# Kernel optimization log

Measured on AMD Instinct MI355X. Metric: run time of the kernel, lower is better.

## Reference

```python
import jax, jax.numpy as jnp
import numpy as np
from jax import lax

B, C, H = 16384, 512, 1024
IN = C + 4  # context + prev_delta(2) + heading(2)
LN_EPS = 1e-5


def _layernorm(x, g, b):
    mu = x.mean(-1, keepdims=True)
    var = ((x - mu) ** 2).mean(-1, keepdims=True)
    return (x - mu) * lax.rsqrt(var + LN_EPS) * g + b


def setup_inputs() -> dict:
    key = jax.random.key(0)
    ks = jax.random.split(key, 16)
    s = lambda fan_in: 1.0 / np.sqrt(fan_in)
    return {
        "context": jax.random.normal(ks[0], (B, C), jnp.float32),
        "last_pos": jax.random.normal(ks[1], (B, 2), jnp.float32),
        "last_delta": jax.random.normal(ks[2], (B, 2), jnp.float32) * 0.1,
        "Wh": jax.random.normal(ks[3], (H, C), jnp.float32) * s(C),
        "bh": jnp.zeros((H,), jnp.float32),
        "Wc": jax.random.normal(ks[4], (H, C), jnp.float32) * s(C),
        "bc": jnp.zeros((H,), jnp.float32),
        "W_ih": jax.random.normal(ks[5], (4 * H, IN), jnp.float32) * s(H),
        "b_ih": jax.random.normal(ks[6], (4 * H,), jnp.float32) * s(H),
        "W_hh": jax.random.normal(ks[7], (4 * H, H), jnp.float32) * s(H),
        "b_hh": jax.random.normal(ks[8], (4 * H,), jnp.float32) * s(H),
        "ln_g": jnp.ones((H,), jnp.float32),
        "ln_b": jnp.zeros((H,), jnp.float32),
        "W1": jax.random.normal(ks[9], (H, H), jnp.float32) * s(H),
        "b1": jnp.zeros((H,), jnp.float32),
        "W2": jax.random.normal(ks[10], (2, H), jnp.float32) * s(H),
        "b2": jnp.zeros((2,), jnp.float32),
        "pred_len": 60,
    }


def reference(context, last_pos, last_delta, Wh, bh, Wc, bc, W_ih, b_ih, W_hh, b_hh,
              ln_g, ln_b, W1, b1, W2, b2, pred_len):
    hidden = jnp.tanh(context @ Wh.T + bh)
    cell = jnp.tanh(context @ Wc.T + bc)
    # context part of LSTM input gates is constant across steps: precompute
    gates_ctx = context @ W_ih[:, :C].T + b_ih  # [B, 4H]
    W_extra = W_ih[:, C:]  # [4H, 4]

    def step(carry, _):
        h, c, pos, pd = carry
        heading = pd / jnp.maximum(jnp.linalg.norm(pd, axis=-1, keepdims=True), 1e-6)
        extra = jnp.concatenate([pd, heading], axis=-1)  # [B,4]
        gates = gates_ctx + extra @ W_extra.T + h @ W_hh.T + b_hh
        i, f, g, o = jnp.split(gates, 4, axis=-1)
        c = jax.nn.sigmoid(f) * c + jax.nn.sigmoid(i) * jnp.tanh(g)
        h = jax.nn.sigmoid(o) * jnp.tanh(c)
        y = _layernorm(h, ln_g, ln_b)  # dropout is identity in eval
        y = jax.nn.gelu(y @ W1.T + b1, approximate=False)
        delta = y @ W2.T + b2  # [B,2]
        pos = pos + delta
        return (h, c, pos, delta), pos

    _, outs = lax.scan(step, (hidden, cell, last_pos, last_delta), None, length=pred_len)
    return jnp.swapaxes(outs, 0, 1)  # [B, pred_len, 2]
```

## Files before the change

### kernel.cpp

```cpp
#include <hip/hip_runtime.h>
#include <math.h>

constexpr int BATCH = 16384;
constexpr int CDIM  = 512;
constexpr int HDIM  = 1024;
constexpr int GDIM  = 4096;
constexpr int TSTEP = 60;
constexpr float LOSC  = 2048.0f;
constexpr float ILOSC = 1.0f / 2048.0f;

typedef _Float16 half_t;
typedef _Float16 halfx8 __attribute__((ext_vector_type(8)));
typedef _Float16 halfx4 __attribute__((ext_vector_type(4)));
typedef float    f32x4  __attribute__((ext_vector_type(4)));
typedef int      i32x4  __attribute__((ext_vector_type(4)));
typedef signed char i8_t;

__device__ __forceinline__ void async_cp16(const void* g, void* l) {
  __builtin_amdgcn_global_load_lds((__attribute__((address_space(1))) void*)g,
                                   (__attribute__((address_space(3))) void*)l,
                                   16, 0, 0);
}

__device__ __forceinline__ half_t hi16(float x) { return (half_t)x; }
__device__ __forceinline__ half_t lo16(float x) {
  return (half_t)((x - (float)((half_t)x)) * LOSC);
}
__device__ __forceinline__ int clamp8(int v) {
  return v > 127 ? 127 : (v < -127 ? -127 : v);
}
__device__ __forceinline__ float sigf(float x) { return 1.0f / (1.0f + expf(-x)); }
__device__ __forceinline__ float geluf(float v) {
  return 0.5f * v * (1.0f + erff(v * 0.70710678118f));
}

__device__ __forceinline__ void swizzle_tiles(int& mt, int& nt) {
  const int gx = gridDim.x, gy = gridDim.y;
  if (gy & 7) { mt = blockIdx.x; nt = blockIdx.y; return; }
  const int lin = blockIdx.y * gx + blockIdx.x;
  const int xcd = lin & 7;
  const int slot = lin >> 3;
  const int npx = gy >> 3;
  nt = xcd * npx + (slot % npx);
  mt = slot / npx;
}

__device__ __forceinline__ void kstep(f32x4 (&acc)[4][4],
    const half_t* __restrict__ A, size_t lda, int krel,
    const half_t* __restrict__ W, size_t ldw, int kw,
    half_t* sA, half_t* sB, int bm0, int bn0) {
  const int tid  = threadIdx.x;
  const int lane = tid & 63;
  const int wave = tid >> 6;
  const int wm = wave >> 1, wn = wave & 1;
  const int ar = lane >> 2;
  const int ak = (lane & 3) * 8;
  const int quad = lane >> 4;
  const int lcol = lane & 15;
#pragma unroll
  for (int cc = 0; cc < 2; ++cc) {
    const int chunk = wave + cc * 4;
    async_cp16(A + (size_t)(bm0 + chunk * 16 + ar) * lda + (krel + ak), sA + chunk * 512);
    async_cp16(W + (size_t)(bn0 + chunk * 16 + ar) * ldw + (kw + ak), sB + chunk * 512);
  }
  asm volatile("s_waitcnt vmcnt(0)" ::: "memory");
  __syncthreads();
  halfx8 af[4], bfr[4];
#pragma unroll
  for (int mi = 0; mi < 4; ++mi)
    af[mi] = *(const halfx8*)&sA[(wm * 64 + mi * 16 + lcol) * 32 + quad * 8];
#pragma unroll
  for (int ni = 0; ni < 4; ++ni)
    bfr[ni] = *(const halfx8*)&sB[(wn * 64 + ni * 16 + lcol) * 32 + quad * 8];
#pragma unroll
  for (int mi = 0; mi < 4; ++mi)
#pragma unroll
    for (int ni = 0; ni < 4; ++ni)
      acc[mi][ni] = __builtin_amdgcn_mfma_f32_16x16x32_f16(af[mi], bfr[ni], acc[mi][ni], 0, 0, 0);
  __syncthreads();
}

__device__ __forceinline__ void scale_acc4(f32x4 (&acc)[4][4], float s) {
#pragma unroll
  for (int i = 0; i < 4; ++i)
#pragma unroll
    for (int j = 0; j < 4; ++j) acc[i][j] *= s;
}

template <int ACT, bool SPLITOUT>
__global__ __launch_bounds__(256, 3)
void gemm3_pre(const half_t* __restrict__ Ahi, const half_t* __restrict__ Alo,
               const half_t* __restrict__ Wcat, const float* __restrict__ bias,
               float* __restrict__ Cf, half_t* __restrict__ Chi,
               half_t* __restrict__ Clo, i8_t* __restrict__ C8, int ldc) {
  __shared__ __align__(16) half_t sA[128 * 32];
  __shared__ __align__(16) half_t sB[128 * 32];
  const int tid = threadIdx.x;
  int mt, nt;
  swizzle_tiles(mt, nt);
  const int bm0 = mt * 128, bn0 = nt * 128;
  f32x4 acc[4][4];
#pragma unroll
  for (int i = 0; i < 4; ++i)
#pragma unroll
    for (int j = 0; j < 4; ++j) acc[i][j] = (f32x4){0.f, 0.f, 0.f, 0.f};
#pragma unroll 1
  for (int k0 = 0; k0 < 512; k0 += 32)
    kstep(acc, Ahi, CDIM, k0, Wcat, 1536, k0, sA, sB, bm0, bn0);
#pragma unroll 1
  for (int k0 = 512; k0 < 1024; k0 += 32)
    kstep(acc, Alo, CDIM, k0 - 512, Wcat, 1536, k0, sA, sB, bm0, bn0);
  scale_acc4(acc, ILOSC);
#pragma unroll 1
  for (int k0 = 1024; k0 < 1536; k0 += 32)
    kstep(acc, Ahi, CDIM, k0 - 1024, Wcat, 1536, k0, sA, sB, bm0, bn0);

  const int lane = tid & 63, wave = tid >> 6;
  const int wm = wave >> 1, wn = wave & 1, quad = lane >> 4, lcol = lane & 15;
#pragma unroll
  for (int ni = 0; ni < 4; ++ni) {
    const int col = bn0 + wn * 64 + ni * 16 + lcol;
    const float bv = bias[col];
#pragma unroll
    for (int mi = 0; mi < 4; ++mi) {
      const int row0 = bm0 + wm * 64 + mi * 16 + quad * 4;
#pragma unroll
      for (int r = 0; r < 4; ++r) {
        float v = acc[mi][ni][r] + bv;
        if (ACT == 1) v = tanhf(v);
        if (SPLITOUT) {
          const size_t idx = (size_t)(row0 + r) * ldc + col;
          const half_t hh = hi16(v);
          const float hiF = (float)hh;
          Chi[idx] = hh;
          Clo[idx] = (half_t)((v - hiF) * LOSC);
          const int hq = clamp8((int)rintf(hiF * 128.0f));
          const int lq = clamp8((int)rintf((v - hiF) * 524288.0f));
          C8[(size_t)(row0 + r) * 2048 + col]        = (i8_t)hq;
          C8[(size_t)(row0 + r) * 2048 + 1024 + col] = (i8_t)lq;
        } else {
          Cf[(size_t)(row0 + r) * ldc + col] = v;
        }
      }
    }
  }
}

__global__ __launch_bounds__(256, 3)
void gemm_gates_cell(const half_t* __restrict__ hAhi, const i8_t* __restrict__ hA8,
                     const half_t* __restrict__ Whh16, const i8_t* __restrict__ Whh8,
                     const int* __restrict__ Ebuf,
                     const float* __restrict__ gctx,
                     const float* __restrict__ dprev, const float* __restrict__ b2,
                     const float* __restrict__ Wxt, float* __restrict__ c,
                     half_t* __restrict__ hBhi, half_t* __restrict__ hBlo,
                     i8_t* __restrict__ hB8, float* __restrict__ statsT) {
  __shared__ __align__(16) unsigned char sAraw[8192];
  __shared__ __align__(16) unsigned char sBraw[8192];
  __shared__ __align__(16) float sE[4][16 * 68];
  const int tid = threadIdx.x;
  const int lane = tid & 63;
  const int wave = tid >> 6;
  const int wm = wave >> 1, wn = wave & 1;
  const int quad = lane >> 4;
  const int lcol = lane & 15;
  int mt, nt;
  swizzle_tiles(mt, nt);
  const int bm0 = mt * 128, bn0 = nt * 128;

  i32x4 acc8[4][4];
#pragma unroll
  for (int i = 0; i < 4; ++i)
#pragma unroll
    for (int j = 0; j < 4; ++j) acc8[i][j] = (i32x4){0, 0, 0, 0};
  {
    const int ar8 = lane >> 2;
    const int ab8 = (lane & 3) * 16;
#pragma unroll 1
    for (int k0 = 0; k0 < 2048; k0 += 64) {
#pragma unroll
      for (int cc = 0; cc < 2; ++cc) {
        const int chunk = wave + cc * 4;
        async_cp16(hA8 + (size_t)(bm0 + chunk * 16 + ar8) * 2048 + (k0 + ab8),
                   sAraw + chunk * 1024);
        async_cp16(Whh8 + (size_t)(bn0 + chunk * 16 + ar8) * 2048 + (k0 + ab8),
                   sBraw + chunk * 1024);
      }
      asm volatile("s_waitcnt vmcnt(0)" ::: "memory");
      __syncthreads();
      i32x4 ai[4], bi[4];
#pragma unroll
      for (int mi = 0; mi < 4; ++mi)
        ai[mi] = *(const i32x4*)&sAraw[(wm * 64 + mi * 16 + lcol) * 64 + quad * 16];
#pragma unroll
      for (int ni = 0; ni < 4; ++ni)
        bi[ni] = *(const i32x4*)&sBraw[(wn * 64 + ni * 16 + lcol) * 64 + quad * 16];
#pragma unroll
      for (int mi = 0; mi < 4; ++mi)
#pragma unroll
        for (int ni = 0; ni < 4; ++ni)
          acc8[mi][ni] = __builtin_amdgcn_mfma_i32_16x16x64_i8(ai[mi], bi[ni], acc8[mi][ni], 0, 0, 0);
      __syncthreads();
    }
  }
  const int E = Ebuf[0];
  f32x4 acc[4][4];
#pragma unroll
  for (int i = 0; i < 4; ++i)
#pragma unroll
    for (int j = 0; j < 4; ++j)
#pragma unroll
      for (int r = 0; r < 4; ++r)
        acc[i][j][r] = ldexpf((float)acc8[i][j][r], E - 25);

#pragma unroll 1
  for (int k0 = 0; k0 < 1024; k0 += 32)
    kstep(acc, hAhi, HDIM, k0, Whh16, 1024, k0,
          (half_t*)sAraw, (half_t*)sBraw, bm0, bn0);

  float* myE = sE[wave];
  const int u = lane & 15;
  const int q = lane >> 4;
  const int j = ((bn0 + wn * 64) >> 2) + u;
  const float b20 = b2[0], b21 = b2[1];
  const float4 wx0 = *(const float4*)(Wxt + (size_t)j * 16 + 0);
  const float4 wx1 = *(const float4*)(Wxt + (size_t)j * 16 + 4);
  const float4 wx2 = *(const float4*)(Wxt + (size_t)j * 16 + 8);
  const float4 wx3 = *(const float4*)(Wxt + (size_t)j * 16 + 12);

#pragma unroll
  for (int mi = 0; mi < 4; ++mi) {
#pragma unroll
    for (int ni = 0; ni < 4; ++ni)
#pragma unroll
      for (int r = 0; r < 4; ++r)
        myE[(quad * 4 + r) * 68 + ni * 16 + lcol] = acc[mi][ni][r];
#pragma unroll
    for (int k = 0; k < 4; ++k) {
      const int rr = q + 4 * k;
      const int row = bm0 + wm * 64 + mi * 16 + rr;
      const f32x4 gv = *(const f32x4*)&myE[rr * 68 + u * 4];
      const float4 gc = *(const float4*)(gctx + (size_t)row * GDIM + 4 * j);
      const float dx = dprev[2 * row] + b20;
      const float dy = dprev[2 * row + 1] + b21;
      const float nrm = fmaxf(sqrtf(dx * dx + dy * dy), 1e-6f);
      const float ex = dx, ey = dy, ehx = dx / nrm, ehy = dy / nrm;
      const float pi = gv[0] + gc.x + ex*wx0.x + ey*wx0.y + ehx*wx0.z + ehy*wx0.w;
      const float pf = gv[1] + gc.y + ex*wx1.x + ey*wx1.y + ehx*wx1.z + ehy*wx1.w;
      const float pg = gv[2] + gc.z + ex*wx2.x + ey*wx2.y + ehx*wx2.z + ehy*wx2.w;
      const float po = gv[3] + gc.w + ex*wx3.x + ey*wx3.y + ehx*wx3.z + ehy*wx3.w;
      const size_t cidx = (size_t)row * HDIM + j;
      const float cn = sigf(pf) * c[cidx] + sigf(pi) * tanhf(pg);
      c[cidx] = cn;
      const float vh = sigf(po) * tanhf(cn);
      const half_t hh = hi16(vh);
      const float hiF = (float)hh;
      hBhi[cidx] = hh;
      hBlo[cidx] = (half_t)((vh - hiF) * LOSC);
      const int hq = clamp8((int)rintf(hiF * 128.0f));
      const int lq = clamp8((int)rintf((vh - hiF) * 524288.0f));
      hB8[(size_t)row * 2048 + j]        = (i8_t)hq;
      hB8[(size_t)row * 2048 + 1024 + j] = (i8_t)lq;
      float ps = vh, pq = vh * vh;
#pragma unroll
      for (int m = 1; m < 16; m <<= 1) {
        ps += __shfl_xor(ps, m, 64);
        pq += __shfl_xor(pq, m, 64);
      }
      if (u == 0) {
        atomicAdd(&statsT[2 * row], ps);
        atomicAdd(&statsT[2 * row + 1], pq);
      }
    }
  }
}

__global__ __launch_bounds__(256, 3)
void gemm_mlp64(const half_t* __restrict__ hBhi, const half_t* __restrict__ hBlo,
                const half_t* __restrict__ W1g, const float* __restrict__ statsT,
                const float* __restrict__ v1, const float* __restrict__ v2,
                const float* __restrict__ W2, float* __restrict__ deltaT) {
  __shared__ __align__(16) half_t sA[128 * 32];
  __shared__ __align__(16) half_t sBl[64 * 32];
  __shared__ __align__(16) half_t sBh[64 * 32];
  const int tid = threadIdx.x;
  const int lane = tid & 63;
  const int wave = tid >> 6;
  const int ar = lane >> 2;
  const int ak = (lane & 3) * 8;
  const int quad = lane >> 4;
  const int lcol = lane & 15;
  int mt, nt;
  swizzle_tiles(mt, nt);
  const int bm0 = mt * 128, bn0 = nt * 64;
  f32x4 accS[2][4], accM[2][4];
#pragma unroll
  for (int i = 0; i < 2; ++i)
#pragma unroll
    for (int jj = 0; jj < 4; ++jj) {
      accS[i][jj] = (f32x4){0.f, 0.f, 0.f, 0.f};
      accM[i][jj] = (f32x4){0.f, 0.f, 0.f, 0.f};
    }

#pragma unroll 1
  for (int k0 = 0; k0 < 1024; k0 += 32) {
#pragma unroll
    for (int cc = 0; cc < 2; ++cc) {
      const int chunk = wave + cc * 4;
      async_cp16(hBhi + (size_t)(bm0 + chunk * 16 + ar) * HDIM + (k0 + ak), sA + chunk * 512);
    }
    async_cp16(W1g + (size_t)(bn0 + wave * 16 + ar) * 2048 + (k0 + ak), sBl + wave * 512);
    async_cp16(W1g + (size_t)(bn0 + wave * 16 + ar) * 2048 + (1024 + k0 + ak), sBh + wave * 512);
    asm volatile("s_waitcnt vmcnt(0)" ::: "memory");
    __syncthreads();
    halfx8 af[2], bl[4], bh[4];
#pragma unroll
    for (int mi = 0; mi < 2; ++mi)
      af[mi] = *(const halfx8*)&sA[(wave * 32 + mi * 16 + lcol) * 32 + quad * 8];
#pragma unroll
    for (int ni = 0; ni < 4; ++ni) {
      bl[ni] = *(const halfx8*)&sBl[(ni * 16 + lcol) * 32 + quad * 8];
      bh[ni] = *(const halfx8*)&sBh[(ni * 16 + lcol) * 32 + quad * 8];
    }
#pragma unroll
    for (int mi = 0; mi < 2; ++mi)
#pragma unroll
      for (int ni = 0; ni < 4; ++ni) {
        accS[mi][ni] = __builtin_amdgcn_mfma_f32_16x16x32_f16(af[mi], bl[ni], accS[mi][ni], 0, 0, 0);
        accM[mi][ni] = __builtin_amdgcn_mfma_f32_16x16x32_f16(af[mi], bh[ni], accM[mi][ni], 0, 0, 0);
      }
    __syncthreads();
  }
#pragma unroll 1
  for (int k0 = 0; k0 < 1024; k0 += 32) {
#pragma unroll
    for (int cc = 0; cc < 2; ++cc) {
      const int chunk = wave + cc * 4;
      async_cp16(hBlo + (size_t)(bm0 + chunk * 16 + ar) * HDIM + (k0 + ak), sA + chunk * 512);
    }
    async_cp16(W1g + (size_t)(bn0 + wave * 16 + ar) * 2048 + (1024 + k0 + ak), sBl + wave * 512);
    asm volatile("s_waitcnt vmcnt(0)" ::: "memory");
    __syncthreads();
    halfx8 af[2], bl[4];
#pragma unroll
    for (int mi = 0; mi < 2; ++mi)
      af[mi] = *(const halfx8*)&sA[(wave * 32 + mi * 16 + lcol) * 32 + quad * 8];
#pragma unroll
    for (int ni = 0; ni < 4; ++ni)
      bl[ni] = *(const halfx8*)&sBl[(ni * 16 + lcol) * 32 + quad * 8];
#pragma unroll
    for (int mi = 0; mi < 2; ++mi)
#pragma unroll
      for (int ni = 0; ni < 4; ++ni)
        accS[mi][ni] = __builtin_amdgcn_mfma_f32_16x16x32_f16(af[mi], bl[ni], accS[mi][ni], 0, 0, 0);
    __syncthreads();
  }
#pragma unroll
  for (int i = 0; i < 2; ++i)
#pragma unroll
    for (int jj = 0; jj < 4; ++jj) accM[i][jj] += accS[i][jj] * ILOSC;

  float w2a[4], w2b[4], v1c[4], v2c[4];
#pragma unroll
  for (int ni = 0; ni < 4; ++ni) {
    const int col = bn0 + ni * 16 + lcol;
    w2a[ni] = W2[col]; w2b[ni] = W2[HDIM + col];
    v1c[ni] = v1[col]; v2c[ni] = v2[col];
  }
#pragma unroll
  for (int mi = 0; mi < 2; ++mi) {
#pragma unroll
    for (int r = 0; r < 4; ++r) {
      const int row = bm0 + wave * 32 + mi * 16 + quad * 4 + r;
      const float S = statsT[2 * row], Q = statsT[2 * row + 1];
      const float mu = S * (1.0f / HDIM);
      const float rs = rsqrtf(Q * (1.0f / HDIM) - mu * mu + 1e-5f);
      float d0 = 0.f, d1 = 0.f;
#pragma unroll
      for (int ni = 0; ni < 4; ++ni) {
        const float g = geluf(rs * (accM[mi][ni][r] - mu * v1c[ni]) + v2c[ni]);
        d0 += g * w2a[ni];
        d1 += g * w2b[ni];
      }
#pragma unroll
      for (int m = 1; m < 16; m <<= 1) {
        d0 += __shfl_xor(d0, m, 64);
        d1 += __shfl_xor(d1, m, 64);
      }
      if (lcol == 0) {
        atomicAdd(&deltaT[2 * row], d0);
        atomicAdd(&deltaT[2 * row + 1], d1);
      }
    }
  }
}

__global__ __launch_bounds__(256)
void write_traj(const float* __restrict__ lp, const float* __restrict__ deltaT,
                const float* __restrict__ b2, float* __restrict__ out, int M) {
  const int b = blockIdx.x * 256 + threadIdx.x;
  if (b >= M) return;
  float px = lp[2 * b], py = lp[2 * b + 1];
  const float b20 = b2[0], b21 = b2[1];
  for (int t = 0; t < TSTEP; ++t) {
    px += deltaT[(size_t)t * M * 2 + 2 * b] + b20;
    py += deltaT[(size_t)t * M * 2 + 2 * b + 1] + b21;
    out[((size_t)b * TSTEP + t) * 2 + 0] = px;
    out[((size_t)b * TSTEP + t) * 2 + 1] = py;
  }
}

__global__ __launch_bounds__(256)
void cvt_split(const float* __restrict__ s, half_t* __restrict__ dhi,
               half_t* __restrict__ dlo, int n4) {
  int i = blockIdx.x * 256 + threadIdx.x;
  if (i >= n4) return;
  const float4 v = ((const float4*)s)[i];
  halfx4 h = { hi16(v.x), hi16(v.y), hi16(v.z), hi16(v.w) };
  halfx4 l = { lo16(v.x), lo16(v.y), lo16(v.z), lo16(v.w) };
  *(halfx4*)(dhi + (size_t)i * 4) = h;
  *(halfx4*)(dlo + (size_t)i * 4) = l;
}

__global__ __launch_bounds__(256)
void wmax_reduce(const float* __restrict__ W, unsigned* __restrict__ mx, int n) {
  float m = 0.f;
  for (int i = blockIdx.x * 256 + threadIdx.x; i < n; i += gridDim.x * 256)
    m = fmaxf(m, fabsf(W[i]));
#pragma unroll
  for (int off = 32; off > 0; off >>= 1)
    m = fmaxf(m, __shfl_down(m, off, 64));
  if ((threadIdx.x & 63) == 0) atomicMax(mx, __float_as_uint(m));
}

__global__ void set_E(const unsigned* __restrict__ mx, int* __restrict__ Ebuf) {
  int e;
  frexpf(__uint_as_float(*mx), &e);
  Ebuf[0] = e - 1;
}

__global__ __launch_bounds__(256)
void build_whh_hyb(const float* __restrict__ Whh, const int* __restrict__ Ebuf,
                   half_t* __restrict__ W16, i8_t* __restrict__ W8) {
  int idx = blockIdx.x * 256 + threadIdx.x;
  if (idx >= GDIM * HDIM) return;
  const int rp = idx >> 10;
  const int k  = idx & 1023;
  const int sr = (rp & 3) * HDIM + (rp >> 2);
  const float w = Whh[(size_t)sr * HDIM + k];
  const half_t whi = (half_t)w;
  const float hiF = (float)whi;
  const float wlo = w - hiF;
  const int E = Ebuf[0];
  W16[(size_t)rp * 1024 + k] = whi;
  W8[(size_t)rp * 2048 + k]        = (i8_t)clamp8((int)rintf(ldexpf(wlo, 18 - E)));
  W8[(size_t)rp * 2048 + 1024 + k] = (i8_t)clamp8((int)rintf(ldexpf(hiF, 6 - E)));
}

__global__ __launch_bounds__(256)
void build_wx(const float* __restrict__ Wih, float* __restrict__ Wxt) {
  int rp = blockIdx.x * 256 + threadIdx.x;
  if (rp >= GDIM) return;
  const int jj = rp >> 2, g = rp & 3;
  const int sr = g * HDIM + jj;
  const float4 v = *(const float4*)(Wih + (size_t)sr * 516 + 512);
  *(float4*)(Wxt + (size_t)jj * 16 + g * 4) = v;
}

__global__ __launch_bounds__(256)
void build_wih_cat(const float* __restrict__ Wih, half_t* __restrict__ dst) {
  int idx = blockIdx.x * 256 + threadIdx.x;
  if (idx >= GDIM * 384) return;
  const int rp = idx / 384;
  const int k  = (idx - rp * 384) * 4;
  const int sr = (rp & 3) * HDIM + (rp >> 2);
  const bool lo = (k < 512);
  const int kk = lo ? k : (k < 1024 ? k - 512 : k - 1024);
  const float4 v = *(const float4*)(Wih + (size_t)sr * 516 + kk);
  half_t* d = dst + (size_t)rp * 1536 + k;
  if (lo) { halfx4 o = { lo16(v.x), lo16(v.y), lo16(v.z), lo16(v.w) }; *(halfx4*)d = o; }
  else    { halfx4 o = { hi16(v.x), hi16(v.y), hi16(v.z), hi16(v.w) }; *(halfx4*)d = o; }
}

__global__ __launch_bounds__(256)
void build_bias(const float* __restrict__ b_ih, const float* __restrict__ b_hh,
                float* __restrict__ bias_i) {
  int rp = blockIdx.x * 256 + threadIdx.x;
  if (rp >= GDIM) return;
  const int sr = (rp & 3) * HDIM + (rp >> 2);
  bias_i[rp] = b_ih[sr] + b_hh[sr];
}

__global__ __launch_bounds__(256)
void build_w1g2(const float* __restrict__ W1, const float* __restrict__ g,
                const float* __restrict__ beta, const float* __restrict__ b1,
                half_t* __restrict__ W1g, float* __restrict__ v1,
                float* __restrict__ v2) {
  const int n = blockIdx.x;
  const int tid = threadIdx.x;
  const int k = tid * 4;
  const float4 w  = *(const float4*)(W1 + (size_t)n * HDIM + k);
  const float4 gg = *(const float4*)(g + k);
  const float4 bb = *(const float4*)(beta + k);
  const float wg0 = w.x*gg.x, wg1 = w.y*gg.y, wg2 = w.z*gg.z, wg3 = w.w*gg.w;
  halfx4 hl = { lo16(wg0), lo16(wg1), lo16(wg2), lo16(wg3) };
  halfx4 hh = { hi16(wg0), hi16(wg1), hi16(wg2), hi16(wg3) };
  *(halfx4*)(W1g + (size_t)n * 2048 + k)        = hl;
  *(halfx4*)(W1g + (size_t)n * 2048 + 1024 + k) = hh;
  float s1 = wg0 + wg1 + wg2 + wg3;
  float s2 = w.x*bb.x + w.y*bb.y + w.z*bb.z + w.w*bb.w;
#pragma unroll
  for (int off = 32; off > 0; off >>= 1) {
    s1 += __shfl_down(s1, off, 64);
    s2 += __shfl_down(s2, off, 64);
  }
  __shared__ float t1[4], t2[4];
  const int wv = tid >> 6, ln = tid & 63;
  if (ln == 0) { t1[wv] = s1; t2[wv] = s2; }
  __syncthreads();
  if (tid == 0) {
    v1[n] = t1[0] + t1[1] + t1[2] + t1[3];
    v2[n] = t2[0] + t2[1] + t2[2] + t2[3] + b1[n];
  }
}

__global__ __launch_bounds__(128)
void build_wc_cat(const float* __restrict__ W, half_t* __restrict__ dst) {
  const int n = blockIdx.x;
  const int k = threadIdx.x * 4;
  const float4 w = *(const float4*)(W + (size_t)n * CDIM + k);
  halfx4 hl = { lo16(w.x), lo16(w.y), lo16(w.z), lo16(w.w) };
  halfx4 hh = { hi16(w.x), hi16(w.y), hi16(w.z), hi16(w.w) };
  *(halfx4*)(dst + (size_t)n * 1536 + k)        = hl;
  *(halfx4*)(dst + (size_t)n * 1536 + 512 + k)  = hh;
  *(halfx4*)(dst + (size_t)n * 1536 + 1024 + k) = hh;
}

__global__ __launch_bounds__(256)
void init_chunk(const float* __restrict__ ld, const float* __restrict__ b2,
                float* __restrict__ delta_init, int M) {
  int b = blockIdx.x * 256 + threadIdx.x;
  if (b >= M) return;
  delta_init[2*b]   = ld[2*b]   - b2[0];
  delta_init[2*b+1] = ld[2*b+1] - b2[1];
}

extern "C" void kernel_launch(void* const* d_in, const int* in_sizes, int n_in,
                              void* d_out, int out_size, void* d_ws, size_t ws_size,
                              hipStream_t stream) {
  const float* context    = (const float*)d_in[0];
  const float* last_pos   = (const float*)d_in[1];
  const float* last_delta = (const float*)d_in[2];
  const float* Wh   = (const float*)d_in[3];
  const float* bh   = (const float*)d_in[4];
  const float* Wc   = (const float*)d_in[5];
  const float* bc   = (const float*)d_in[6];
  const float* W_ih = (const float*)d_in[7];
  const float* b_ih = (const float*)d_in[8];
  const float* W_hh = (const float*)d_in[9];
  const float* b_hh = (const float*)d_in[10];
  const float* ln_g = (const float*)d_in[11];
  const float* ln_b = (const float*)d_in[12];
  const float* W1   = (const float*)d_in[13];
  const float* b1   = (const float*)d_in[14];
  const float* W2   = (const float*)d_in[15];
  const float* b2   = (const float*)d_in[16];
  float* out = (float*)d_out;

  const size_t stat_bytes =
      (size_t)GDIM * 1024 * 2 +
      (size_t)GDIM * 2048 +
      (size_t)GDIM * 1536 * 2 +
      (size_t)HDIM * 2048 * 2 +
      2 * (size_t)HDIM * 1536 * 2 +
      (size_t)HDIM * 16 * 4 + (size_t)GDIM * 4 + 2 * (size_t)HDIM * 4 + 32768;
  int NC = 0;
  for (int nc : {2, 4, 8, 16}) {
    const size_t M = BATCH / nc;
    const size_t chunk_bytes = 4 * M * HDIM * 2 +
                               2 * M * 2048 +
                               2 * M * CDIM * 2 +
                               M * HDIM * 4 +
                               (size_t)M * GDIM * 4 +
                               M * 2 * 4 +
                               2 * (size_t)TSTEP * M * 2 * 4 + 32768;
    if (stat_bytes + chunk_bytes <= ws_size) { NC = nc; break; }
  }
  if (NC == 0) return;
  const int M = BATCH / NC;

  char* w = (char*)d_ws;
  auto take = [&](size_t bytes) {
    char* p = w;
    w += (bytes + 255) & ~(size_t)255;
    return p;
  };
  half_t* Whh16   = (half_t*)take((size_t)GDIM * 1024 * 2);
  i8_t*   Whh8    = (i8_t*)take((size_t)GDIM * 2048);
  half_t* Wih_cat = (half_t*)take((size_t)GDIM * 1536 * 2);
  half_t* W1g2    = (half_t*)take((size_t)HDIM * 2048 * 2);
  half_t* Wh_cat  = (half_t*)take((size_t)HDIM * 1536 * 2);
  half_t* Wc_cat  = (half_t*)take((size_t)HDIM * 1536 * 2);
  float*  Wxt     = (float*)take((size_t)HDIM * 16 * 4);
  float*  bias_i  = (float*)take((size_t)GDIM * 4);
  float*  v1      = (float*)take((size_t)HDIM * 4);
  float*  v2      = (float*)take((size_t)HDIM * 4);
  unsigned* mx    = (unsigned*)take(256);
  int*    Ebuf    = (int*)take(256);
  half_t* h0hi    = (half_t*)take((size_t)M * HDIM * 2);
  half_t* h0lo    = (half_t*)take((size_t)M * HDIM * 2);
  half_t* h1hi    = (half_t*)take((size_t)M * HDIM * 2);
  half_t* h1lo    = (half_t*)take((size_t)M * HDIM * 2);
  i8_t*   h08     = (i8_t*)take((size_t)M * 2048);
  i8_t*   h18     = (i8_t*)take((size_t)M * 2048);
  half_t* ctx_hi  = (half_t*)take((size_t)M * CDIM * 2);
  half_t* ctx_lo  = (half_t*)take((size_t)M * CDIM * 2);
  float*  c_f     = (float*)take((size_t)M * HDIM * 4);
  float*  gctx    = (float*)take((size_t)M * GDIM * 4);
  float*  dinit   = (float*)take((size_t)M * 2 * 4);
  const size_t sd_bytes = 2 * (size_t)TSTEP * M * 2 * 4;
  float*  statsAll = (float*)take(sd_bytes);
  float*  deltaAll = statsAll + (size_t)TSTEP * M * 2;

  hipMemsetAsync(mx, 0, 4, stream);
  wmax_reduce<<<256, 256, 0, stream>>>(W_hh, mx, GDIM * HDIM);
  set_E<<<1, 1, 0, stream>>>(mx, Ebuf);
  build_whh_hyb<<<(GDIM * HDIM + 255) / 256, 256, 0, stream>>>(W_hh, Ebuf, Whh16, Whh8);
  build_wx<<<(GDIM + 255) / 256, 256, 0, stream>>>(W_ih, Wxt);
  build_wih_cat<<<(GDIM * 384 + 255) / 256, 256, 0, stream>>>(W_ih, Wih_cat);
  build_bias<<<(GDIM + 255) / 256, 256, 0, stream>>>(b_ih, b_hh, bias_i);
  build_w1g2<<<HDIM, 256, 0, stream>>>(W1, ln_g, ln_b, b1, W1g2, v1, v2);
  build_wc_cat<<<HDIM, 128, 0, stream>>>(Wh, Wh_cat);
  build_wc_cat<<<HDIM, 128, 0, stream>>>(Wc, Wc_cat);

  const dim3 blk(256);
  for (int chunk = 0; chunk < NC; ++chunk) {
    const size_t base = (size_t)chunk * M;
    hipMemsetAsync(statsAll, 0, sd_bytes, stream);
    cvt_split<<<(M * CDIM / 4 + 255) / 256, 256, 0, stream>>>(
        context + base * CDIM, ctx_hi, ctx_lo, M * CDIM / 4);
    gemm3_pre<1, true ><<<dim3(M/128, HDIM/128), blk, 0, stream>>>(
        ctx_hi, ctx_lo, Wh_cat, bh, nullptr, h0hi, h0lo, h08, HDIM);
    gemm3_pre<1, false><<<dim3(M/128, HDIM/128), blk, 0, stream>>>(
        ctx_hi, ctx_lo, Wc_cat, bc, c_f, nullptr, nullptr, nullptr, HDIM);
    gemm3_pre<0, false><<<dim3(M/128, GDIM/128), blk, 0, stream>>>(
        ctx_hi, ctx_lo, Wih_cat, bias_i, gctx, nullptr, nullptr, nullptr, GDIM);
    init_chunk<<<(M + 255) / 256, 256, 0, stream>>>(
        last_delta + base * 2, b2, dinit, M);

    const half_t* hAhi = h0hi; const half_t* hAlo = h0lo;
    const i8_t* hA8 = h08;
    half_t* hBhi = h1hi; half_t* hBlo = h1lo;
    i8_t* hB8 = h18;
    for (int t = 0; t < TSTEP; ++t) {
      const float* dprev = (t == 0) ? dinit : deltaAll + (size_t)(t - 1) * M * 2;
      gemm_gates_cell<<<dim3(M/128, GDIM/128), blk, 0, stream>>>(
          hAhi, hA8, Whh16, Whh8, Ebuf, gctx, dprev, b2, Wxt, c_f,
          hBhi, hBlo, hB8, statsAll + (size_t)t * M * 2);
      gemm_mlp64<<<dim3(M/128, HDIM/64), blk, 0, stream>>>(
          hBhi, hBlo, W1g2, statsAll + (size_t)t * M * 2, v1, v2, W2,
          deltaAll + (size_t)t * M * 2);
      half_t* th = hBhi; hBhi = (half_t*)hAhi; hAhi = th;
      half_t* tl = hBlo; hBlo = (half_t*)hAlo; hAlo = tl;
      i8_t* t8 = hB8; hB8 = (i8_t*)hA8; hA8 = t8;
    }
    write_traj<<<(M + 255) / 256, 256, 0, stream>>>(
        last_pos + base * 2, deltaAll, b2, out + base * TSTEP * 2, M);
  }
  (void)in_sizes; (void)n_in; (void)out_size;
}
```

Measured before the change: 38.79 ms.

## Use hybrid int8 split-precision GEMM for the MLP W1 product, drop fp16 lo buffers

The per-step MLP GEMM previously ran three fp16 MFMA passes (hi*lo, lo*hi, hi*hi) over hidden and W1 split into fp16 hi/lo parts. It now computes the correction terms with a single int8 MFMA pass over concatenated int8 hi/lo quantizations, then adds one fp16 hi*hi pass. W1 is quantized with a shared exponent derived from a new max-reduction. This removes the fp16 lo hidden buffers and their writes each step, cutting memory traffic and MFMA work, at the cost of some precision in the correction terms.

```diff
diff --git a/kernel.cpp b/kernel.cpp
--- a/kernel.cpp
+++ b/kernel.cpp
@@ -92,7 +92,7 @@
 void gemm3_pre(const half_t* __restrict__ Ahi, const half_t* __restrict__ Alo,
                const half_t* __restrict__ Wcat, const float* __restrict__ bias,
                float* __restrict__ Cf, half_t* __restrict__ Chi,
-               half_t* __restrict__ Clo, i8_t* __restrict__ C8, int ldc) {
+               i8_t* __restrict__ C8, int ldc) {
   __shared__ __align__(16) half_t sA[128 * 32];
   __shared__ __align__(16) half_t sB[128 * 32];
   const int tid = threadIdx.x;
@@ -129,11 +129,9 @@
         float v = acc[mi][ni][r] + bv;
         if (ACT == 1) v = tanhf(v);
         if (SPLITOUT) {
-          const size_t idx = (size_t)(row0 + r) * ldc + col;
           const half_t hh = hi16(v);
           const float hiF = (float)hh;
-          Chi[idx] = hh;
-          Clo[idx] = (half_t)((v - hiF) * LOSC);
+          Chi[(size_t)(row0 + r) * ldc + col] = hh;
           const int hq = clamp8((int)rintf(hiF * 128.0f));
           const int lq = clamp8((int)rintf((v - hiF) * 524288.0f));
           C8[(size_t)(row0 + r) * 2048 + col]        = (i8_t)hq;
@@ -153,8 +151,8 @@
                      const float* __restrict__ gctx,
                      const float* __restrict__ dprev, const float* __restrict__ b2,
                      const float* __restrict__ Wxt, float* __restrict__ c,
-                     half_t* __restrict__ hBhi, half_t* __restrict__ hBlo,
-                     i8_t* __restrict__ hB8, float* __restrict__ statsT) {
+                     half_t* __restrict__ hBhi, i8_t* __restrict__ hB8,
+                     float* __restrict__ statsT) {
   __shared__ __align__(16) unsigned char sAraw[8192];
   __shared__ __align__(16) unsigned char sBraw[8192];
   __shared__ __align__(16) float sE[4][16 * 68];
@@ -256,7 +254,6 @@
       const half_t hh = hi16(vh);
       const float hiF = (float)hh;
       hBhi[cidx] = hh;
-      hBlo[cidx] = (half_t)((vh - hiF) * LOSC);
       const int hq = clamp8((int)rintf(hiF * 128.0f));
       const int lq = clamp8((int)rintf((vh - hiF) * 524288.0f));
       hB8[(size_t)row * 2048 + j]        = (i8_t)hq;
@@ -276,89 +273,97 @@
 }
 
 __global__ __launch_bounds__(256, 3)
-void gemm_mlp64(const half_t* __restrict__ hBhi, const half_t* __restrict__ hBlo,
-                const half_t* __restrict__ W1g, const float* __restrict__ statsT,
+void gemm_mlp64(const half_t* __restrict__ hBhi, const i8_t* __restrict__ hB8,
+                const half_t* __restrict__ W1hi, const i8_t* __restrict__ W18,
+                const int* __restrict__ Ebuf, const float* __restrict__ statsT,
                 const float* __restrict__ v1, const float* __restrict__ v2,
                 const float* __restrict__ W2, float* __restrict__ deltaT) {
-  __shared__ __align__(16) half_t sA[128 * 32];
-  __shared__ __align__(16) half_t sBl[64 * 32];
-  __shared__ __align__(16) half_t sBh[64 * 32];
+  __shared__ __align__(16) unsigned char sAraw[8192];
+  __shared__ __align__(16) unsigned char sBraw[4096];
   const int tid = threadIdx.x;
   const int lane = tid & 63;
   const int wave = tid >> 6;
-  const int ar = lane >> 2;
-  const int ak = (lane & 3) * 8;
   const int quad = lane >> 4;
   const int lcol = lane & 15;
   int mt, nt;
   swizzle_tiles(mt, nt);
   const int bm0 = mt * 128, bn0 = nt * 64;
-  f32x4 accS[2][4], accM[2][4];
+
+  i32x4 acc8[2][4];
 #pragma unroll
   for (int i = 0; i < 2; ++i)
 #pragma unroll
-    for (int jj = 0; jj < 4; ++jj) {
-      accS[i][jj] = (f32x4){0.f, 0.f, 0.f, 0.f};
-      accM[i][jj] = (f32x4){0.f, 0.f, 0.f, 0.f};
+    for (int jj = 0; jj < 4; ++jj) acc8[i][jj] = (i32x4){0, 0, 0, 0};
+  {
+    const int ar8 = lane >> 2;
+    const int ab8 = (lane & 3) * 16;
+#pragma unroll 1
+    for (int k0 = 0; k0 < 2048; k0 += 64) {
+#pragma unroll
+      for (int cc = 0; cc < 2; ++cc) {
+        const int chunk = wave + cc * 4;
+        async_cp16(hB8 + (size_t)(bm0 + chunk * 16 + ar8) * 2048 + (k0 + ab8),
+                   sAraw + chunk * 1024);
+      }
+      async_cp16(W18 + (size_t)(bn0 + wave * 16 + ar8) * 2048 + (k0 + ab8),
+                 sBraw + wave * 1024);
+      asm volatile("s_waitcnt vmcnt(0)" ::: "memory");
+      __syncthreads();
+      i32x4 ai[2], bi[4];
+#pragma unroll
+      for (int mi = 0; mi < 2; ++mi)
+        ai[mi] = *(const i32x4*)&sAraw[(wave * 32 + mi * 16 + lcol) * 64 + quad * 16];
+#pragma unroll
+      for (int ni = 0; ni < 4; ++ni)
+        bi[ni] = *(const i32x4*)&sBraw[(ni * 16 + lcol) * 64 + quad * 16];
+#pragma unroll
+      for (int mi = 0; mi < 2; ++mi)
+#pragma unroll
+        for (int ni = 0; ni < 4; ++ni)
+          acc8[mi][ni] = __builtin_amdgcn_mfma_i32_16x16x64_i8(ai[mi], bi[ni], acc8[mi][ni], 0, 0, 0);
+      __syncthreads();
     }
-
+  }
+  const int E1 = Ebuf[1];
+  f32x4 accM[2][4];
+#pragma unroll
+  for (int i = 0; i < 2; ++i)
+#pragma unroll
+    for (int jj = 0; jj < 4; ++jj)
+#pragma unroll
+      for (int r = 0; r < 4; ++r)
+        accM[i][jj][r] = ldexpf((float)acc8[i][jj][r], E1 - 25);
+
+  {
+    half_t* sA = (half_t*)sAraw;
+    half_t* sB = (half_t*)sBraw;
+    const int ar = lane >> 2;
+    const int ak = (lane & 3) * 8;
 #pragma unroll 1
-  for (int k0 = 0; k0 < 1024; k0 += 32) {
-#pragma unroll
-    for (int cc = 0; cc < 2; ++cc) {
-      const int chunk = wave + cc * 4;
-      async_cp16(hBhi + (size_t)(bm0 + chunk * 16 + ar) * HDIM + (k0 + ak), sA + chunk * 512);
+    for (int k0 = 0; k0 < 1024; k0 += 32) {
+#pragma unroll
+      for (int cc = 0; cc < 2; ++cc) {
+        const int chunk = wave + cc * 4;
+        async_cp16(hBhi + (size_t)(bm0 + chunk * 16 + ar) * HDIM + (k0 + ak), sA + chunk * 512);
+      }
+      async_cp16(W1hi + (size_t)(bn0 + wave * 16 + ar) * HDIM + (k0 + ak), sB + wave * 512);
+      asm volatile("s_waitcnt vmcnt(0)" ::: "memory");
+      __syncthreads();
+      halfx8 af[2], bfr[4];
+#pragma unroll
+      for (int mi = 0; mi < 2; ++mi)
+        af[mi] = *(const halfx8*)&sA[(wave * 32 + mi * 16 + lcol) * 32 + quad * 8];
+#pragma unroll
+      for (int ni = 0; ni < 4; ++ni)
+        bfr[ni] = *(const halfx8*)&sB[(ni * 16 + lcol) * 32 + quad * 8];
+#pragma unroll
+      for (int mi = 0; mi < 2; ++mi)
+#pragma unroll
+        for (int ni = 0; ni < 4; ++ni)
+          accM[mi][ni] = __builtin_amdgcn_mfma_f32_16x16x32_f16(af[mi], bfr[ni], accM[mi][ni], 0, 0, 0);
+      __syncthreads();
     }
-    async_cp16(W1g + (size_t)(bn0 + wave * 16 + ar) * 2048 + (k0 + ak), sBl + wave * 512);
-    async_cp16(W1g + (size_t)(bn0 + wave * 16 + ar) * 2048 + (1024 + k0 + ak), sBh + wave * 512);
-    asm volatile("s_waitcnt vmcnt(0)" ::: "memory");
-    __syncthreads();
-    halfx8 af[2], bl[4], bh[4];
-#pragma unroll
-    for (int mi = 0; mi < 2; ++mi)
-      af[mi] = *(const halfx8*)&sA[(wave * 32 + mi * 16 + lcol) * 32 + quad * 8];
-#pragma unroll
-    for (int ni = 0; ni < 4; ++ni) {
-      bl[ni] = *(const halfx8*)&sBl[(ni * 16 + lcol) * 32 + quad * 8];
-      bh[ni] = *(const halfx8*)&sBh[(ni * 16 + lcol) * 32 + quad * 8];
-    }
-#pragma unroll
-    for (int mi = 0; mi < 2; ++mi)
-#pragma unroll
-      for (int ni = 0; ni < 4; ++ni) {
-        accS[mi][ni] = __builtin_amdgcn_mfma_f32_16x16x32_f16(af[mi], bl[ni], accS[mi][ni], 0, 0, 0);
-        accM[mi][ni] = __builtin_amdgcn_mfma_f32_16x16x32_f16(af[mi], bh[ni], accM[mi][ni], 0, 0, 0);
-      }
-    __syncthreads();
-  }
-#pragma unroll 1
-  for (int k0 = 0; k0 < 1024; k0 += 32) {
-#pragma unroll
-    for (int cc = 0; cc < 2; ++cc) {
-      const int chunk = wave + cc * 4;
-      async_cp16(hBlo + (size_t)(bm0 + chunk * 16 + ar) * HDIM + (k0 + ak), sA + chunk * 512);
-    }
-    async_cp16(W1g + (size_t)(bn0 + wave * 16 + ar) * 2048 + (1024 + k0 + ak), sBl + wave * 512);
-    asm volatile("s_waitcnt vmcnt(0)" ::: "memory");
-    __syncthreads();
-    halfx8 af[2], bl[4];
-#pragma unroll
-    for (int mi = 0; mi < 2; ++mi)
-      af[mi] = *(const halfx8*)&sA[(wave * 32 + mi * 16 + lcol) * 32 + quad * 8];
-#pragma unroll
-    for (int ni = 0; ni < 4; ++ni)
-      bl[ni] = *(const halfx8*)&sBl[(ni * 16 + lcol) * 32 + quad * 8];
-#pragma unroll
-    for (int mi = 0; mi < 2; ++mi)
-#pragma unroll
-      for (int ni = 0; ni < 4; ++ni)
-        accS[mi][ni] = __builtin_amdgcn_mfma_f32_16x16x32_f16(af[mi], bl[ni], accS[mi][ni], 0, 0, 0);
-    __syncthreads();
-  }
-#pragma unroll
-  for (int i = 0; i < 2; ++i)
-#pragma unroll
-    for (int jj = 0; jj < 4; ++jj) accM[i][jj] += accS[i][jj] * ILOSC;
+  }
 
   float w2a[4], w2b[4], v1c[4], v2c[4];
 #pragma unroll
@@ -433,10 +438,24 @@
   if ((threadIdx.x & 63) == 0) atomicMax(mx, __float_as_uint(m));
 }
 
+__global__ __launch_bounds__(256)
+void wmax_w1g(const float* __restrict__ W1, const float* __restrict__ g,
+              unsigned* __restrict__ mx) {
+  float m = 0.f;
+  for (int i = blockIdx.x * 256 + threadIdx.x; i < HDIM * HDIM; i += gridDim.x * 256)
+    m = fmaxf(m, fabsf(W1[i] * g[i & 1023]));
+#pragma unroll
+  for (int off = 32; off > 0; off >>= 1)
+    m = fmaxf(m, __shfl_down(m, off, 64));
+  if ((threadIdx.x & 63) == 0) atomicMax(mx, __float_as_uint(m));
+}
+
 __global__ void set_E(const unsigned* __restrict__ mx, int* __restrict__ Ebuf) {
   int e;
-  frexpf(__uint_as_float(*mx), &e);
+  frexpf(__uint_as_float(mx[0]), &e);
   Ebuf[0] = e - 1;
+  frexpf(__uint_as_float(mx[1]), &e);
+  Ebuf[1] = e - 1;
 }
 
 __global__ __launch_bounds__(256)
@@ -458,6 +477,49 @@
 }
 
 __global__ __launch_bounds__(256)
+void build_w1_hyb(const float* __restrict__ W1, const float* __restrict__ g,
+                  const float* __restrict__ beta, const float* __restrict__ b1,
+                  const int* __restrict__ Ebuf, half_t* __restrict__ W1hi,
+                  i8_t* __restrict__ W18, float* __restrict__ v1,
+                  float* __restrict__ v2) {
+  const int n = blockIdx.x;
+  const int tid = threadIdx.x;
+  const int k = tid * 4;
+  const int E1 = Ebuf[1];
+  const float4 w  = *(const float4*)(W1 + (size_t)n * HDIM + k);
+  const float4 gg = *(const float4*)(g + k);
+  const float4 bb = *(const float4*)(beta + k);
+  float wg[4] = { w.x*gg.x, w.y*gg.y, w.z*gg.z, w.w*gg.w };
+  halfx4 hh;
+  float s1 = 0.f;
+#pragma unroll
+  for (int u = 0; u < 4; ++u) {
+    const half_t h = (half_t)wg[u];
+    hh[u] = h;
+    const float hiF = (float)h;
+    const float lo = wg[u] - hiF;
+    W18[(size_t)n * 2048 + k + u]        = (i8_t)clamp8((int)rintf(ldexpf(lo, 18 - E1)));
+    W18[(size_t)n * 2048 + 1024 + k + u] = (i8_t)clamp8((int)rintf(ldexpf(hiF, 6 - E1)));
+    s1 += wg[u];
+  }
+  *(halfx4*)(W1hi + (size_t)n * HDIM + k) = hh;
+  float s2 = w.x*bb.x + w.y*bb.y + w.z*bb.z + w.w*bb.w;
+#pragma unroll
+  for (int off = 32; off > 0; off >>= 1) {
+    s1 += __shfl_down(s1, off, 64);
+    s2 += __shfl_down(s2, off, 64);
+  }
+  __shared__ float t1[4], t2[4];
+  const int wv = tid >> 6, ln = tid & 63;
+  if (ln == 0) { t1[wv] = s1; t2[wv] = s2; }
+  __syncthreads();
+  if (tid == 0) {
+    v1[n] = t1[0] + t1[1] + t1[2] + t1[3];
+    v2[n] = t2[0] + t2[1] + t2[2] + t2[3] + b1[n];
+  }
+}
+
+__global__ __launch_bounds__(256)
 void build_wx(const float* __restrict__ Wih, float* __restrict__ Wxt) {
   int rp = blockIdx.x * 256 + threadIdx.x;
   if (rp >= GDIM) return;
@@ -489,39 +551,6 @@
   if (rp >= GDIM) return;
   const int sr = (rp & 3) * HDIM + (rp >> 2);
   bias_i[rp] = b_ih[sr] + b_hh[sr];
-}
-
-__global__ __launch_bounds__(256)
-void build_w1g2(const float* __restrict__ W1, const float* __restrict__ g,
-                const float* __restrict__ beta, const float* __restrict__ b1,
-                half_t* __restrict__ W1g, float* __restrict__ v1,
-                float* __restrict__ v2) {
-  const int n = blockIdx.x;
-  const int tid = threadIdx.x;
-  const int k = tid * 4;
-  const float4 w  = *(const float4*)(W1 + (size_t)n * HDIM + k);
-  const float4 gg = *(const float4*)(g + k);
-  const float4 bb = *(const float4*)(beta + k);
-  const float wg0 = w.x*gg.x, wg1 = w.y*gg.y, wg2 = w.z*gg.z, wg3 = w.w*gg.w;
-  halfx4 hl = { lo16(wg0), lo16(wg1), lo16(wg2), lo16(wg3) };
-  halfx4 hh = { hi16(wg0), hi16(wg1), hi16(wg2), hi16(wg3) };
-  *(halfx4*)(W1g + (size_t)n * 2048 + k)        = hl;
-  *(halfx4*)(W1g + (size_t)n * 2048 + 1024 + k) = hh;
-  float s1 = wg0 + wg1 + wg2 + wg3;
-  float s2 = w.x*bb.x + w.y*bb.y + w.z*bb.z + w.w*bb.w;
-#pragma unroll
-  for (int off = 32; off > 0; off >>= 1) {
-    s1 += __shfl_down(s1, off, 64);
-    s2 += __shfl_down(s2, off, 64);
-  }
-  __shared__ float t1[4], t2[4];
-  const int wv = tid >> 6, ln = tid & 63;
-  if (ln == 0) { t1[wv] = s1; t2[wv] = s2; }
-  __syncthreads();
-  if (tid == 0) {
-    v1[n] = t1[0] + t1[1] + t1[2] + t1[3];
-    v2[n] = t2[0] + t2[1] + t2[2] + t2[3] + b1[n];
-  }
 }
 
 __global__ __launch_bounds__(128)
@@ -571,13 +600,14 @@
       (size_t)GDIM * 1024 * 2 +
       (size_t)GDIM * 2048 +
       (size_t)GDIM * 1536 * 2 +
-      (size_t)HDIM * 2048 * 2 +
+      (size_t)HDIM * 1024 * 2 +
+      (size_t)HDIM * 2048 +
       2 * (size_t)HDIM * 1536 * 2 +
       (size_t)HDIM * 16 * 4 + (size_t)GDIM * 4 + 2 * (size_t)HDIM * 4 + 32768;
   int NC = 0;
   for (int nc : {2, 4, 8, 16}) {
     const size_t M = BATCH / nc;
-    const size_t chunk_bytes = 4 * M * HDIM * 2 +
+    const size_t chunk_bytes = 2 * M * HDIM * 2 +
                                2 * M * 2048 +
                                2 * M * CDIM * 2 +
                                M * HDIM * 4 +
@@ -598,7 +628,8 @@
   half_t* Whh16   = (half_t*)take((size_t)GDIM * 1024 * 2);
   i8_t*   Whh8    = (i8_t*)take((size_t)GDIM * 2048);
   half_t* Wih_cat = (half_t*)take((size_t)GDIM * 1536 * 2);
-  half_t* W1g2    = (half_t*)take((size_t)HDIM * 2048 * 2);
+  half_t* W1hi    = (half_t*)take((size_t)HDIM * 1024 * 2);
+  i8_t*   W18     = (i8_t*)take((size_t)HDIM * 2048);
   half_t* Wh_cat  = (half_t*)take((size_t)HDIM * 1536 * 2);
   half_t* Wc_cat  = (half_t*)take((size_t)HDIM * 1536 * 2);
   float*  Wxt     = (float*)take((size_t)HDIM * 16 * 4);
@@ -608,9 +639,7 @@
   unsigned* mx    = (unsigned*)take(256);
   int*    Ebuf    = (int*)take(256);
   half_t* h0hi    = (half_t*)take((size_t)M * HDIM * 2);
-  half_t* h0lo    = (half_t*)take((size_t)M * HDIM * 2);
   half_t* h1hi    = (half_t*)take((size_t)M * HDIM * 2);
-  half_t* h1lo    = (half_t*)take((size_t)M * HDIM * 2);
   i8_t*   h08     = (i8_t*)take((size_t)M * 2048);
   i8_t*   h18     = (i8_t*)take((size_t)M * 2048);
   half_t* ctx_hi  = (half_t*)take((size_t)M * CDIM * 2);
@@ -622,14 +651,15 @@
   float*  statsAll = (float*)take(sd_bytes);
   float*  deltaAll = statsAll + (size_t)TSTEP * M * 2;
 
-  hipMemsetAsync(mx, 0, 4, stream);
+  hipMemsetAsync(mx, 0, 8, stream);
   wmax_reduce<<<256, 256, 0, stream>>>(W_hh, mx, GDIM * HDIM);
+  wmax_w1g<<<256, 256, 0, stream>>>(W1, ln_g, mx + 1);
   set_E<<<1, 1, 0, stream>>>(mx, Ebuf);
   build_whh_hyb<<<(GDIM * HDIM + 255) / 256, 256, 0, stream>>>(W_hh, Ebuf, Whh16, Whh8);
+  build_w1_hyb<<<HDIM, 256, 0, stream>>>(W1, ln_g, ln_b, b1, Ebuf, W1hi, W18, v1, v2);
   build_wx<<<(GDIM + 255) / 256, 256, 0, stream>>>(W_ih, Wxt);
   build_wih_cat<<<(GDIM * 384 + 255) / 256, 256, 0, stream>>>(W_ih, Wih_cat);
   build_bias<<<(GDIM + 255) / 256, 256, 0, stream>>>(b_ih, b_hh, bias_i);
-  build_w1g2<<<HDIM, 256, 0, stream>>>(W1, ln_g, ln_b, b1, W1g2, v1, v2);
   build_wc_cat<<<HDIM, 128, 0, stream>>>(Wh, Wh_cat);
   build_wc_cat<<<HDIM, 128, 0, stream>>>(Wc, Wc_cat);
 
@@ -640,28 +670,27 @@
     cvt_split<<<(M * CDIM / 4 + 255) / 256, 256, 0, stream>>>(
         context + base * CDIM, ctx_hi, ctx_lo, M * CDIM / 4);
     gemm3_pre<1, true ><<<dim3(M/128, HDIM/128), blk, 0, stream>>>(
-        ctx_hi, ctx_lo, Wh_cat, bh, nullptr, h0hi, h0lo, h08, HDIM);
+        ctx_hi, ctx_lo, Wh_cat, bh, nullptr, h0hi, h08, HDIM);
     gemm3_pre<1, false><<<dim3(M/128, HDIM/128), blk, 0, stream>>>(
-        ctx_hi, ctx_lo, Wc_cat, bc, c_f, nullptr, nullptr, nullptr, HDIM);
+        ctx_hi, ctx_lo, Wc_cat, bc, c_f, nullptr, nullptr, HDIM);
     gemm3_pre<0, false><<<dim3(M/128, GDIM/128), blk, 0, stream>>>(
-        ctx_hi, ctx_lo, Wih_cat, bias_i, gctx, nullptr, nullptr, nullptr, GDIM);
+        ctx_hi, ctx_lo, Wih_cat, bias_i, gctx, nullptr, nullptr, GDIM);
     init_chunk<<<(M + 255) / 256, 256, 0, stream>>>(
         last_delta + base * 2, b2, dinit, M);
 
-    const half_t* hAhi = h0hi; const half_t* hAlo = h0lo;
+    const half_t* hAhi = h0hi;
     const i8_t* hA8 = h08;
-    half_t* hBhi = h1hi; half_t* hBlo = h1lo;
+    half_t* hBhi = h1hi;
     i8_t* hB8 = h18;
     for (int t = 0; t < TSTEP; ++t) {
       const float* dprev = (t == 0) ? dinit : deltaAll + (size_t)(t - 1) * M * 2;
       gemm_gates_cell<<<dim3(M/128, GDIM/128), blk, 0, stream>>>(
           hAhi, hA8, Whh16, Whh8, Ebuf, gctx, dprev, b2, Wxt, c_f,
-          hBhi, hBlo, hB8, statsAll + (size_t)t * M * 2);
+          hBhi, hB8, statsAll + (size_t)t * M * 2);
       gemm_mlp64<<<dim3(M/128, HDIM/64), blk, 0, stream>>>(
-          hBhi, hBlo, W1g2, statsAll + (size_t)t * M * 2, v1, v2, W2,
+          hBhi, hB8, W1hi, W18, Ebuf, statsAll + (size_t)t * M * 2, v1, v2, W2,
           deltaAll + (size_t)t * M * 2);
       half_t* th = hBhi; hBhi = (half_t*)hAhi; hAhi = th;
-      half_t* tl = hBlo; hBlo = (half_t*)hAlo; hAlo = tl;
       i8_t* t8 = hB8; hB8 = (i8_t*)hA8; hA8 = t8;
     }
     write_traj<<<(M + 255) / 256, 256, 0, stream>>>(
```

After: 36.32 ms. -6.4%, faster.
